# Kernel tuning notes

Measured on AMD Instinct MI355X. Metric: run time of the kernel, lower is better.

The kernel has to match this reference:

```python
import jax, jax.numpy as jnp
import numpy as np

D_MODEL = 1024
NUM_HEADS = 16
D_K = D_MODEL // NUM_HEADS


def setup_inputs() -> dict:
    key = jax.random.key(0)
    ks = jax.random.split(key, 11)
    B, S, D = 4, 2048, D_MODEL
    scale = 1.0 / np.sqrt(D)
    inp = {
        'query': jax.random.normal(ks[0], (B, S, D), jnp.float32),
        'key':   jax.random.normal(ks[1], (B, S, D), jnp.float32),
        'value': jax.random.normal(ks[2], (B, S, D), jnp.float32),
        'Wq': jax.random.normal(ks[3], (D, D), jnp.float32) * scale,
        'bq': jnp.zeros((D,), jnp.float32),
        'Wk': jax.random.normal(ks[4], (D, D), jnp.float32) * scale,
        'bk': jnp.zeros((D,), jnp.float32),
        'Wv': jax.random.normal(ks[5], (D, D), jnp.float32) * scale,
        'bv': jnp.zeros((D,), jnp.float32),
        'Wo': jax.random.normal(ks[6], (D, D), jnp.float32) * scale,
        'bo': jnp.zeros((D,), jnp.float32),
    }
    return inp


def _mha(query, key, value, Wq, bq, Wk, bk, Wv, bv, Wo, bo):
    B, S, D = query.shape
    H, dk = NUM_HEADS, D_K
    # Linear projections then split heads: [B, S, D] -> [B, H, S, dk]
    def split_heads(x):
        return x.reshape(B, S, H, dk).transpose(0, 2, 1, 3)
    Q = split_heads(query @ Wq + bq)
    K = split_heads(key @ Wk + bk)
    V = split_heads(value @ Wv + bv)
    # Scores: [B, H, S, S]
    scores = jnp.einsum('bhqd,bhkd->bhqk', Q, K) / jnp.sqrt(jnp.float32(dk)).astype(Q.dtype)
    attn = jax.nn.softmax(scores, axis=-1)
    # Context: [B, H, S, dk] -> [B, S, D]
    ctx = jnp.einsum('bhqk,bhkd->bhqd', attn, V)
    ctx = ctx.transpose(0, 2, 1, 3).reshape(B, S, D)
    return ctx @ Wo + bo


def reference(query, key, value, Wq, bq, Wk, bk, Wv, bv, Wo, bo):
    return _mha(query, key, value, Wq, bq, Wk, bk, Wv, bv, Wo, bo)
```

## Files before the change

kernel.cpp:

```cpp
#include <hip/hip_runtime.h>

typedef __attribute__((ext_vector_type(8))) short s8v;
typedef __attribute__((ext_vector_type(4))) float f4v;

#define MFMA16(a, b, c) __builtin_amdgcn_mfma_f32_16x16x32_bf16(a, b, c, 0, 0, 0)

__device__ __forceinline__ unsigned short f2bf(float f) {
    union { float f; unsigned int u; } v; v.f = f;
    unsigned int u = v.u;
    unsigned int r = (u + 0x7FFFu + ((u >> 16) & 1u)) >> 16;
    return (unsigned short)r;
}

__device__ __forceinline__ unsigned int cvt_pk_bf16(float lo, float hi) {
    unsigned int r;
    asm volatile("v_cvt_pk_bf16_f32 %0, %1, %2" : "=v"(r) : "v"(lo), "v"(hi));
    return r;
}

__device__ __forceinline__ void gl16(const void* g, void* l) {
    __builtin_amdgcn_global_load_lds(
        (const __attribute__((address_space(1))) void*)g,
        (__attribute__((address_space(3))) void*)l, 16, 0, 0);
}

__global__ __launch_bounds__(256) void cvt_bf16_k(
        const float* __restrict__ X0, const float* __restrict__ X1,
        const float* __restrict__ X2,
        unsigned short* __restrict__ Y0, unsigned short* __restrict__ Y1,
        unsigned short* __restrict__ Y2) {
    const float* X; unsigned short* Y;
    switch (blockIdx.y) {
        case 0:  X = X0; Y = Y0; break;
        case 1:  X = X1; Y = Y1; break;
        default: X = X2; Y = Y2; break;
    }
    size_t i = ((size_t)blockIdx.x * 256 + threadIdx.x) * 8;
    float4 a = *reinterpret_cast<const float4*>(X + i);
    float4 b = *reinterpret_cast<const float4*>(X + i + 4);
    s8v o;
    o[0] = (short)f2bf(a.x); o[1] = (short)f2bf(a.y);
    o[2] = (short)f2bf(a.z); o[3] = (short)f2bf(a.w);
    o[4] = (short)f2bf(b.x); o[5] = (short)f2bf(b.y);
    o[6] = (short)f2bf(b.z); o[7] = (short)f2bf(b.w);
    *reinterpret_cast<s8v*>(Y + i) = o;
}

__global__ __launch_bounds__(256) void transpose_cvt_k(
        const float* __restrict__ W0, const float* __restrict__ W1,
        const float* __restrict__ W2, const float* __restrict__ W3,
        unsigned short* __restrict__ T0, unsigned short* __restrict__ T1,
        unsigned short* __restrict__ T2, unsigned short* __restrict__ T3) {
    __shared__ float tile[32][33];
    const float* W; unsigned short* T;
    switch (blockIdx.z) {
        case 0:  W = W0; T = T0; break;
        case 1:  W = W1; T = T1; break;
        case 2:  W = W2; T = T2; break;
        default: W = W3; T = T3; break;
    }
    int tx = threadIdx.x & 31, ty = threadIdx.x >> 5;
    int k0 = blockIdx.x * 32, n0 = blockIdx.y * 32;
#pragma unroll
    for (int i = 0; i < 32; i += 8)
        tile[ty + i][tx] = W[(size_t)(k0 + ty + i) * 1024 + n0 + tx];
    __syncthreads();
#pragma unroll
    for (int i = 0; i < 32; i += 8)
        T[(size_t)(n0 + ty + i) * 1024 + k0 + tx] = f2bf(tile[tx][ty + i]);
}

template <int OUT_MODE>
__global__ __launch_bounds__(256, 2) void gemm_bt_k(
        const unsigned short* __restrict__ A, const unsigned short* __restrict__ Bt,
        const float* __restrict__ bias, void* __restrict__ C) {
    constexpr int Kd = 1024, Nd = 1024;
    __shared__ __attribute__((aligned(16))) unsigned short As[128 * 32];
    __shared__ __attribute__((aligned(16))) unsigned short Bs[128 * 32];

    const int tid  = threadIdx.x;
    const int lane = tid & 63, wave = tid >> 6;
    const int g = lane >> 4, li = lane & 15;
    const int wr = wave >> 1, wc = wave & 1;
    const int row0 = blockIdx.y * 128, col0 = blockIdx.x * 128;
    const int lrow = lane >> 2, lcol = (lane & 3) * 8;

    f4v acc[4][4];
#pragma unroll
    for (int m = 0; m < 4; m++)
#pragma unroll
        for (int n = 0; n < 4; n++) acc[m][n] = (f4v){0.f, 0.f, 0.f, 0.f};

    for (int kt = 0; kt < Kd; kt += 32) {
        __syncthreads();
#pragma unroll
        for (int jj = 0; jj < 2; jj++) {
            int j = wave * 2 + jj;
            gl16(A  + (size_t)(row0 + j * 16 + lrow) * Kd + kt + lcol, &As[j * 512]);
            gl16(Bt + (size_t)(col0 + j * 16 + lrow) * Kd + kt + lcol, &Bs[j * 512]);
        }
        __syncthreads();

        s8v af[4], bf[4];
#pragma unroll
        for (int m = 0; m < 4; m++)
            af[m] = *reinterpret_cast<const s8v*>(&As[(wr * 64 + m * 16 + li) * 32 + g * 8]);
#pragma unroll
        for (int n = 0; n < 4; n++)
            bf[n] = *reinterpret_cast<const s8v*>(&Bs[(wc * 64 + n * 16 + li) * 32 + g * 8]);
        __builtin_amdgcn_s_setprio(1);
#pragma unroll
        for (int m = 0; m < 4; m++)
#pragma unroll
            for (int n = 0; n < 4; n++)
                acc[m][n] = MFMA16(af[m], bf[n], acc[m][n]);
        __builtin_amdgcn_s_setprio(0);
    }

#pragma unroll
    for (int n = 0; n < 4; n++) {
        int col = col0 + wc * 64 + n * 16 + li;
        float bv = bias[col];
#pragma unroll
        for (int m = 0; m < 4; m++) {
            int rbase = row0 + wr * 64 + m * 16 + g * 4;
            if constexpr (OUT_MODE == 2) {
                int h = col >> 6, d = col & 63;
                int b = rbase >> 11, s = rbase & 2047;
                ushort4 pk;
                pk.x = f2bf(acc[m][n][0] + bv);
                pk.y = f2bf(acc[m][n][1] + bv);
                pk.z = f2bf(acc[m][n][2] + bv);
                pk.w = f2bf(acc[m][n][3] + bv);
                *reinterpret_cast<ushort4*>(
                    (unsigned short*)C + ((((size_t)b * 16 + h) * 64 + d) * 2048 + s)) = pk;
            } else {
#pragma unroll
                for (int r = 0; r < 4; r++) {
                    float v = acc[m][n][r] + bv;
                    if constexpr (OUT_MODE == 1)
                        ((float*)C)[(size_t)(rbase + r) * Nd + col] = v;
                    else
                        ((unsigned short*)C)[(size_t)(rbase + r) * Nd + col] = f2bf(v);
                }
            }
        }
    }
}

__global__ __launch_bounds__(256, 2) void attn_k(
        const unsigned short* __restrict__ Q, const unsigned short* __restrict__ K,
        const unsigned short* __restrict__ Vt, unsigned short* __restrict__ Ctx) {
    constexpr int S = 2048, Dm = 1024, DKh = 64;
    constexpr int LDK = 72, LDV = 136, LDP = 40;
    constexpr float CEXP = 0.125f * 1.44269504f;
    __shared__ __attribute__((aligned(16))) unsigned short K_lds[128 * LDK];
    __shared__ __attribute__((aligned(16))) unsigned short V_lds[64 * LDV];
    __shared__ __attribute__((aligned(16))) unsigned short P_lds[4][32 * LDP];

    const int tid  = threadIdx.x;
    const int lane = tid & 63, wave = tid >> 6;
    const int g = lane >> 4, li = lane & 15;
    const int id = blockIdx.x;
    const int bh = (id & 7) * 8 + ((id >> 3) & 7);
    const int qp = id >> 6;
    const int b = bh >> 4, h = bh & 15;
    const size_t base  = (size_t)b * S * Dm + (size_t)h * DKh;
    const size_t vbase = (size_t)bh * DKh * S;
    const int q00 = qp * 256 + wave * 32;

    s8v qf[2][2][2];
#pragma unroll
    for (int qt = 0; qt < 2; qt++)
#pragma unroll
        for (int rb = 0; rb < 2; rb++)
#pragma unroll
            for (int ks = 0; ks < 2; ks++)
                qf[qt][rb][ks] = *reinterpret_cast<const s8v*>(
                        Q + base + (size_t)(q00 + qt * 128 + rb * 16 + li) * Dm
                           + ks * 32 + g * 8);

    f4v octx[2][2][4];
    float m_run[2][2][4], l_run[2][2][4];
#pragma unroll
    for (int qt = 0; qt < 2; qt++)
#pragma unroll
        for (int rb = 0; rb < 2; rb++) {
#pragma unroll
            for (int nb = 0; nb < 4; nb++) octx[qt][rb][nb] = (f4v){0.f, 0.f, 0.f, 0.f};
#pragma unroll
            for (int r = 0; r < 4; r++) { m_run[qt][rb][r] = -1e30f; l_run[qt][rb][r] = 0.f; }
        }

    const int rdswz = ((li >> 2) & 3) << 3;

    for (int t = 0; t < 16; t++) {
        const int kv0 = t * 128;
        __syncthreads();
#pragma unroll
        for (int i = 0; i < 4; i++) {
            int e = (i * 256 + tid) * 8;
            int s = e >> 6, d = e & 63;
            *reinterpret_cast<s8v*>(&K_lds[s * LDK + d]) =
                *reinterpret_cast<const s8v*>(K + base + (size_t)(kv0 + s) * Dm + d);
            int dv = e >> 7, sv = e & 127;
            *reinterpret_cast<s8v*>(&V_lds[dv * LDV + sv]) =
                *reinterpret_cast<const s8v*>(Vt + vbase + (size_t)dv * S + kv0 + sv);
        }
        __syncthreads();

#pragma unroll
        for (int qt = 0; qt < 2; qt++) {
            f4v sc[2][8];
#pragma unroll
            for (int rb = 0; rb < 2; rb++)
#pragma unroll
                for (int cb = 0; cb < 8; cb++) sc[rb][cb] = (f4v){0.f, 0.f, 0.f, 0.f};
            __builtin_amdgcn_s_setprio(1);
#pragma unroll
            for (int cb = 0; cb < 8; cb++) {
#pragma unroll
                for (int ks = 0; ks < 2; ks++) {
                    s8v kf = *reinterpret_cast<const s8v*>(
                            &K_lds[(cb * 16 + li) * LDK + ks * 32 + g * 8]);
                    sc[0][cb] = MFMA16(qf[qt][0][ks], kf, sc[0][cb]);
                    sc[1][cb] = MFMA16(qf[qt][1][ks], kf, sc[1][cb]);
                }
            }
            __builtin_amdgcn_s_setprio(0);

            float rsum[2][4];
#pragma unroll
            for (int rb = 0; rb < 2; rb++) {
                float rmax[4];
#pragma unroll
                for (int r = 0; r < 4; r++) {
                    float v = sc[rb][0][r];
#pragma unroll
                    for (int cb = 1; cb < 8; cb++) v = fmaxf(v, sc[rb][cb][r]);
                    rmax[r] = v * CEXP;
                }
#pragma unroll
                for (int mask = 1; mask < 16; mask <<= 1)
#pragma unroll
                    for (int r = 0; r < 4; r++)
                        rmax[r] = fmaxf(rmax[r], __shfl_xor(rmax[r], mask, 64));
#pragma unroll
                for (int r = 0; r < 4; r++) {
                    float mn = fmaxf(m_run[qt][rb][r], rmax[r]);
                    float scl = __builtin_amdgcn_exp2f(m_run[qt][rb][r] - mn);
                    m_run[qt][rb][r] = mn;
                    l_run[qt][rb][r] *= scl;
                    rsum[rb][r] = 0.f;
#pragma unroll
                    for (int nb = 0; nb < 4; nb++) octx[qt][rb][nb][r] *= scl;
                }
            }

#pragma unroll
            for (int ks = 0; ks < 4; ks++) {
#pragma unroll
                for (int rb = 0; rb < 2; rb++) {
#pragma unroll
                    for (int cc = 0; cc < 2; cc++) {
                        int cb = ks * 2 + cc;
                        float p0 = __builtin_amdgcn_exp2f(fmaf(sc[rb][cb][0], CEXP, -m_run[qt][rb][0]));
                        float p1 = __builtin_amdgcn_exp2f(fmaf(sc[rb][cb][1], CEXP, -m_run[qt][rb][1]));
                        float p2 = __builtin_amdgcn_exp2f(fmaf(sc[rb][cb][2], CEXP, -m_run[qt][rb][2]));
                        float p3 = __builtin_amdgcn_exp2f(fmaf(sc[rb][cb][3], CEXP, -m_run[qt][rb][3]));
                        rsum[rb][0] += p0; rsum[rb][1] += p1;
                        rsum[rb][2] += p2; rsum[rb][3] += p3;
                        unsigned int u01 = cvt_pk_bf16(p0, p1);
                        unsigned int u23 = cvt_pk_bf16(p2, p3);
                        int rowb = rb * 16 + g * 4;
                        int colS = (cc * 16 + li) ^ (g << 3);
                        P_lds[wave][(rowb + 0) * LDP + colS] = (unsigned short)u01;
                        P_lds[wave][(rowb + 1) * LDP + colS] = (unsigned short)(u01 >> 16);
                        P_lds[wave][(rowb + 2) * LDP + colS] = (unsigned short)u23;
                        P_lds[wave][(rowb + 3) * LDP + colS] = (unsigned short)(u23 >> 16);
                    }
                }
                s8v vf[4], pf[2];
#pragma unroll
                for (int nb = 0; nb < 4; nb++)
                    vf[nb] = *reinterpret_cast<const s8v*>(
                            &V_lds[(nb * 16 + li) * LDV + ks * 32 + g * 8]);
#pragma unroll
                for (int rb = 0; rb < 2; rb++)
                    pf[rb] = *reinterpret_cast<const s8v*>(
                            &P_lds[wave][(rb * 16 + li) * LDP + ((g * 8) ^ rdswz)]);
                __builtin_amdgcn_s_setprio(1);
#pragma unroll
                for (int rb = 0; rb < 2; rb++)
#pragma unroll
                    for (int nb = 0; nb < 4; nb++)
                        octx[qt][rb][nb] = MFMA16(pf[rb], vf[nb], octx[qt][rb][nb]);
                __builtin_amdgcn_s_setprio(0);
            }

#pragma unroll
            for (int mask = 1; mask < 16; mask <<= 1)
#pragma unroll
                for (int rb = 0; rb < 2; rb++)
#pragma unroll
                    for (int r = 0; r < 4; r++)
                        rsum[rb][r] += __shfl_xor(rsum[rb][r], mask, 64);
#pragma unroll
            for (int rb = 0; rb < 2; rb++)
#pragma unroll
                for (int r = 0; r < 4; r++) l_run[qt][rb][r] += rsum[rb][r];
        }
    }

#pragma unroll
    for (int qt = 0; qt < 2; qt++)
#pragma unroll
        for (int rb = 0; rb < 2; rb++)
#pragma unroll
            for (int r = 0; r < 4; r++) {
                float inv = 1.0f / l_run[qt][rb][r];
                int row = q00 + qt * 128 + rb * 16 + g * 4 + r;
#pragma unroll
                for (int nb = 0; nb < 4; nb++) {
                    int d = nb * 16 + li;
                    Ctx[base + (size_t)row * Dm + d] = f2bf(octx[qt][rb][nb][r] * inv);
                }
            }
}

extern "C" void kernel_launch(void* const* d_in, const int* in_sizes, int n_in,
                              void* d_out, int out_size, void* d_ws, size_t ws_size,
                              hipStream_t stream) {
    const float* query = (const float*)d_in[0];
    const float* key   = (const float*)d_in[1];
    const float* value = (const float*)d_in[2];
    const float* Wq = (const float*)d_in[3];
    const float* bq = (const float*)d_in[4];
    const float* Wk = (const float*)d_in[5];
    const float* bk = (const float*)d_in[6];
    const float* Wv = (const float*)d_in[7];
    const float* bv = (const float*)d_in[8];
    const float* Wo = (const float*)d_in[9];
    const float* bo = (const float*)d_in[10];

    unsigned short* ws = (unsigned short*)d_ws;
    const size_t MD = (size_t)8192 * 1024;
    unsigned short* Qb  = ws;
    unsigned short* Kb  = Qb + MD;
    unsigned short* Vtb = Kb + MD;
    unsigned short* Cb  = Vtb + MD;
    unsigned short* Qx  = Cb + MD;
    unsigned short* Kx  = Qx + MD;
    unsigned short* Vx  = Kx + MD;
    unsigned short* Wqt = Vx + MD;
    unsigned short* Wkt = Wqt + 1024 * 1024;
    unsigned short* Wvt = Wkt + 1024 * 1024;
    unsigned short* Wot = Wvt + 1024 * 1024;

    cvt_bf16_k<<<dim3(4096, 3), 256, 0, stream>>>(query, key, value, Qx, Kx, Vx);
    transpose_cvt_k<<<dim3(32, 32, 4), 256, 0, stream>>>(Wq, Wk, Wv, Wo, Wqt, Wkt, Wvt, Wot);
    gemm_bt_k<0><<<dim3(8, 64), 256, 0, stream>>>(Qx, Wqt, bq, Qb);
    gemm_bt_k<0><<<dim3(8, 64), 256, 0, stream>>>(Kx, Wkt, bk, Kb);
    gemm_bt_k<2><<<dim3(8, 64), 256, 0, stream>>>(Vx, Wvt, bv, Vtb);
    attn_k<<<512, 256, 0, stream>>>(Qb, Kb, Vtb, Cb);
    gemm_bt_k<1><<<dim3(8, 64), 256, 0, stream>>>(Cb, Wot, bo, (float*)d_out);
}
```

Measured before the change: 300.3 us.

## Merge QKV GEMMs into one launch and shrink attention tiles for occupancy

The three projection GEMMs become one launch with blockIdx.z selecting Q, K or V, which removes launch gaps and fills more CUs (1536 blocks instead of 512 per launch). The attention kernel now gives each block 128 queries instead of 256 and steps through KV in chunks of 64 instead of 128. This doubles the grid to 1024 blocks, shrinks LDS and register use, and raises launch bounds to 4 blocks per CU to improve latency hiding. The cost is twice as many K/V tile loads per query and twice as many barriers and softmax rescale steps.

```diff
diff --git a/kernel.cpp b/kernel.cpp
--- a/kernel.cpp
+++ b/kernel.cpp
@@ -71,18 +71,15 @@
 }
 
 template <int OUT_MODE>
-__global__ __launch_bounds__(256, 2) void gemm_bt_k(
+__device__ __forceinline__ void gemm_body(
         const unsigned short* __restrict__ A, const unsigned short* __restrict__ Bt,
-        const float* __restrict__ bias, void* __restrict__ C) {
+        const float* __restrict__ bias, void* __restrict__ C,
+        unsigned short* As, unsigned short* Bs, int row0, int col0) {
     constexpr int Kd = 1024, Nd = 1024;
-    __shared__ __attribute__((aligned(16))) unsigned short As[128 * 32];
-    __shared__ __attribute__((aligned(16))) unsigned short Bs[128 * 32];
-
     const int tid  = threadIdx.x;
     const int lane = tid & 63, wave = tid >> 6;
     const int g = lane >> 4, li = lane & 15;
     const int wr = wave >> 1, wc = wave & 1;
-    const int row0 = blockIdx.y * 128, col0 = blockIdx.x * 128;
     const int lrow = lane >> 2, lcol = (lane & 3) * 8;
 
     f4v acc[4][4];
@@ -148,14 +145,42 @@
     }
 }
 
-__global__ __launch_bounds__(256, 2) void attn_k(
+__global__ __launch_bounds__(256, 2) void qkv_gemm_k(
+        const unsigned short* __restrict__ Qx, const unsigned short* __restrict__ Kx,
+        const unsigned short* __restrict__ Vx,
+        const unsigned short* __restrict__ Wqt, const unsigned short* __restrict__ Wkt,
+        const unsigned short* __restrict__ Wvt,
+        const float* __restrict__ bq, const float* __restrict__ bk,
+        const float* __restrict__ bv,
+        unsigned short* __restrict__ Qb, unsigned short* __restrict__ Kb,
+        unsigned short* __restrict__ Vtb) {
+    __shared__ __attribute__((aligned(16))) unsigned short As[128 * 32];
+    __shared__ __attribute__((aligned(16))) unsigned short Bs[128 * 32];
+    const int row0 = blockIdx.y * 128, col0 = blockIdx.x * 128;
+    switch (blockIdx.z) {
+        case 0:  gemm_body<0>(Qx, Wqt, bq, Qb,  As, Bs, row0, col0); break;
+        case 1:  gemm_body<0>(Kx, Wkt, bk, Kb,  As, Bs, row0, col0); break;
+        default: gemm_body<2>(Vx, Wvt, bv, Vtb, As, Bs, row0, col0); break;
+    }
+}
+
+__global__ __launch_bounds__(256, 2) void out_gemm_k(
+        const unsigned short* __restrict__ A, const unsigned short* __restrict__ Bt,
+        const float* __restrict__ bias, float* __restrict__ C) {
+    __shared__ __attribute__((aligned(16))) unsigned short As[128 * 32];
+    __shared__ __attribute__((aligned(16))) unsigned short Bs[128 * 32];
+    gemm_body<1>(A, Bt, bias, C, As, Bs, blockIdx.y * 128, blockIdx.x * 128);
+}
+
+__global__ __launch_bounds__(256, 4) void attn_k(
         const unsigned short* __restrict__ Q, const unsigned short* __restrict__ K,
         const unsigned short* __restrict__ Vt, unsigned short* __restrict__ Ctx) {
     constexpr int S = 2048, Dm = 1024, DKh = 64;
-    constexpr int LDK = 72, LDV = 136, LDP = 40;
+    constexpr int KVB = 64, NT = S / KVB;
+    constexpr int LDK = 72, LDV = 72, LDP = 40;
     constexpr float CEXP = 0.125f * 1.44269504f;
-    __shared__ __attribute__((aligned(16))) unsigned short K_lds[128 * LDK];
-    __shared__ __attribute__((aligned(16))) unsigned short V_lds[64 * LDV];
+    __shared__ __attribute__((aligned(16))) unsigned short K_lds[KVB * LDK];
+    __shared__ __attribute__((aligned(16))) unsigned short V_lds[DKh * LDV];
     __shared__ __attribute__((aligned(16))) unsigned short P_lds[4][32 * LDP];
 
     const int tid  = threadIdx.x;
@@ -163,169 +188,158 @@
     const int g = lane >> 4, li = lane & 15;
     const int id = blockIdx.x;
     const int bh = (id & 7) * 8 + ((id >> 3) & 7);
-    const int qp = id >> 6;
+    const int qt = id >> 6;
     const int b = bh >> 4, h = bh & 15;
+    const int q0 = qt * 128 + wave * 32;
     const size_t base  = (size_t)b * S * Dm + (size_t)h * DKh;
     const size_t vbase = (size_t)bh * DKh * S;
-    const int q00 = qp * 256 + wave * 32;
-
-    s8v qf[2][2][2];
-#pragma unroll
-    for (int qt = 0; qt < 2; qt++)
-#pragma unroll
-        for (int rb = 0; rb < 2; rb++)
-#pragma unroll
-            for (int ks = 0; ks < 2; ks++)
-                qf[qt][rb][ks] = *reinterpret_cast<const s8v*>(
-                        Q + base + (size_t)(q00 + qt * 128 + rb * 16 + li) * Dm
-                           + ks * 32 + g * 8);
-
-    f4v octx[2][2][4];
-    float m_run[2][2][4], l_run[2][2][4];
-#pragma unroll
-    for (int qt = 0; qt < 2; qt++)
-#pragma unroll
-        for (int rb = 0; rb < 2; rb++) {
-#pragma unroll
-            for (int nb = 0; nb < 4; nb++) octx[qt][rb][nb] = (f4v){0.f, 0.f, 0.f, 0.f};
-#pragma unroll
-            for (int r = 0; r < 4; r++) { m_run[qt][rb][r] = -1e30f; l_run[qt][rb][r] = 0.f; }
-        }
+
+    s8v qf[2][2];
+#pragma unroll
+    for (int rb = 0; rb < 2; rb++)
+#pragma unroll
+        for (int ks = 0; ks < 2; ks++)
+            qf[rb][ks] = *reinterpret_cast<const s8v*>(
+                    Q + base + (size_t)(q0 + rb * 16 + li) * Dm + ks * 32 + g * 8);
+
+    f4v octx[2][4];
+    float m_run[2][4], l_run[2][4];
+#pragma unroll
+    for (int rb = 0; rb < 2; rb++) {
+#pragma unroll
+        for (int nb = 0; nb < 4; nb++) octx[rb][nb] = (f4v){0.f, 0.f, 0.f, 0.f};
+#pragma unroll
+        for (int r = 0; r < 4; r++) { m_run[rb][r] = -1e30f; l_run[rb][r] = 0.f; }
+    }
 
     const int rdswz = ((li >> 2) & 3) << 3;
 
-    for (int t = 0; t < 16; t++) {
-        const int kv0 = t * 128;
+    for (int t = 0; t < NT; t++) {
+        const int kv0 = t * KVB;
         __syncthreads();
 #pragma unroll
-        for (int i = 0; i < 4; i++) {
+        for (int i = 0; i < 2; i++) {
             int e = (i * 256 + tid) * 8;
             int s = e >> 6, d = e & 63;
             *reinterpret_cast<s8v*>(&K_lds[s * LDK + d]) =
                 *reinterpret_cast<const s8v*>(K + base + (size_t)(kv0 + s) * Dm + d);
-            int dv = e >> 7, sv = e & 127;
-            *reinterpret_cast<s8v*>(&V_lds[dv * LDV + sv]) =
-                *reinterpret_cast<const s8v*>(Vt + vbase + (size_t)dv * S + kv0 + sv);
+            *reinterpret_cast<s8v*>(&V_lds[s * LDV + d]) =
+                *reinterpret_cast<const s8v*>(Vt + vbase + (size_t)s * S + kv0 + d);
         }
         __syncthreads();
 
-#pragma unroll
-        for (int qt = 0; qt < 2; qt++) {
-            f4v sc[2][8];
+        f4v sc[2][4];
+#pragma unroll
+        for (int rb = 0; rb < 2; rb++)
+#pragma unroll
+            for (int cb = 0; cb < 4; cb++) sc[rb][cb] = (f4v){0.f, 0.f, 0.f, 0.f};
+        __builtin_amdgcn_s_setprio(1);
+#pragma unroll
+        for (int cb = 0; cb < 4; cb++) {
+#pragma unroll
+            for (int ks = 0; ks < 2; ks++) {
+                s8v kf = *reinterpret_cast<const s8v*>(
+                        &K_lds[(cb * 16 + li) * LDK + ks * 32 + g * 8]);
+                sc[0][cb] = MFMA16(qf[0][ks], kf, sc[0][cb]);
+                sc[1][cb] = MFMA16(qf[1][ks], kf, sc[1][cb]);
+            }
+        }
+        __builtin_amdgcn_s_setprio(0);
+
+        float rsum[2][4];
+#pragma unroll
+        for (int rb = 0; rb < 2; rb++) {
+            float rmax[4];
+#pragma unroll
+            for (int r = 0; r < 4; r++) {
+                float v = sc[rb][0][r];
+#pragma unroll
+                for (int cb = 1; cb < 4; cb++) v = fmaxf(v, sc[rb][cb][r]);
+                rmax[r] = v * CEXP;
+            }
+#pragma unroll
+            for (int mask = 1; mask < 16; mask <<= 1)
+#pragma unroll
+                for (int r = 0; r < 4; r++)
+                    rmax[r] = fmaxf(rmax[r], __shfl_xor(rmax[r], mask, 64));
+#pragma unroll
+            for (int r = 0; r < 4; r++) {
+                float mn = fmaxf(m_run[rb][r], rmax[r]);
+                float scl = __builtin_amdgcn_exp2f(m_run[rb][r] - mn);
+                m_run[rb][r] = mn;
+                l_run[rb][r] *= scl;
+                rsum[rb][r] = 0.f;
+#pragma unroll
+                for (int nb = 0; nb < 4; nb++) octx[rb][nb][r] *= scl;
+            }
+        }
+
+#pragma unroll
+        for (int ks = 0; ks < 2; ks++) {
+#pragma unroll
+            for (int rb = 0; rb < 2; rb++) {
+#pragma unroll
+                for (int cc = 0; cc < 2; cc++) {
+                    int cb = ks * 2 + cc;
+                    float p0 = __builtin_amdgcn_exp2f(fmaf(sc[rb][cb][0], CEXP, -m_run[rb][0]));
+                    float p1 = __builtin_amdgcn_exp2f(fmaf(sc[rb][cb][1], CEXP, -m_run[rb][1]));
+                    float p2 = __builtin_amdgcn_exp2f(fmaf(sc[rb][cb][2], CEXP, -m_run[rb][2]));
+                    float p3 = __builtin_amdgcn_exp2f(fmaf(sc[rb][cb][3], CEXP, -m_run[rb][3]));
+                    rsum[rb][0] += p0; rsum[rb][1] += p1;
+                    rsum[rb][2] += p2; rsum[rb][3] += p3;
+                    unsigned int u01 = cvt_pk_bf16(p0, p1);
+                    unsigned int u23 = cvt_pk_bf16(p2, p3);
+                    int rowb = rb * 16 + g * 4;
+                    int colS = (cc * 16 + li) ^ (g << 3);
+                    P_lds[wave][(rowb + 0) * LDP + colS] = (unsigned short)u01;
+                    P_lds[wave][(rowb + 1) * LDP + colS] = (unsigned short)(u01 >> 16);
+                    P_lds[wave][(rowb + 2) * LDP + colS] = (unsigned short)u23;
+                    P_lds[wave][(rowb + 3) * LDP + colS] = (unsigned short)(u23 >> 16);
+                }
+            }
+            s8v vf[4], pf[2];
+#pragma unroll
+            for (int nb = 0; nb < 4; nb++)
+                vf[nb] = *reinterpret_cast<const s8v*>(
+                        &V_lds[(nb * 16 + li) * LDV + ks * 32 + g * 8]);
 #pragma unroll
             for (int rb = 0; rb < 2; rb++)
-#pragma unroll
-                for (int cb = 0; cb < 8; cb++) sc[rb][cb] = (f4v){0.f, 0.f, 0.f, 0.f};
+                pf[rb] = *reinterpret_cast<const s8v*>(
+                        &P_lds[wave][(rb * 16 + li) * LDP + ((g * 8) ^ rdswz)]);
             __builtin_amdgcn_s_setprio(1);
 #pragma unroll
-            for (int cb = 0; cb < 8; cb++) {
-#pragma unroll
-                for (int ks = 0; ks < 2; ks++) {
-                    s8v kf = *reinterpret_cast<const s8v*>(
-                            &K_lds[(cb * 16 + li) * LDK + ks * 32 + g * 8]);
-                    sc[0][cb] = MFMA16(qf[qt][0][ks], kf, sc[0][cb]);
-                    sc[1][cb] = MFMA16(qf[qt][1][ks], kf, sc[1][cb]);
-                }
-            }
+            for (int rb = 0; rb < 2; rb++)
+#pragma unroll
+                for (int nb = 0; nb < 4; nb++)
+                    octx[rb][nb] = MFMA16(pf[rb], vf[nb], octx[rb][nb]);
             __builtin_amdgcn_s_setprio(0);
-
-            float rsum[2][4];
-#pragma unroll
-            for (int rb = 0; rb < 2; rb++) {
-                float rmax[4];
-#pragma unroll
-                for (int r = 0; r < 4; r++) {
-                    float v = sc[rb][0][r];
-#pragma unroll
-                    for (int cb = 1; cb < 8; cb++) v = fmaxf(v, sc[rb][cb][r]);
-                    rmax[r] = v * CEXP;
-                }
-#pragma unroll
-                for (int mask = 1; mask < 16; mask <<= 1)
-#pragma unroll
-                    for (int r = 0; r < 4; r++)
-                        rmax[r] = fmaxf(rmax[r], __shfl_xor(rmax[r], mask, 64));
-#pragma unroll
-                for (int r = 0; r < 4; r++) {
-                    float mn = fmaxf(m_run[qt][rb][r], rmax[r]);
-                    float scl = __builtin_amdgcn_exp2f(m_run[qt][rb][r] - mn);
-                    m_run[qt][rb][r] = mn;
-                    l_run[qt][rb][r] *= scl;
-                    rsum[rb][r] = 0.f;
-#pragma unroll
-                    for (int nb = 0; nb < 4; nb++) octx[qt][rb][nb][r] *= scl;
-                }
-            }
-
-#pragma unroll
-            for (int ks = 0; ks < 4; ks++) {
-#pragma unroll
-                for (int rb = 0; rb < 2; rb++) {
-#pragma unroll
-                    for (int cc = 0; cc < 2; cc++) {
-                        int cb = ks * 2 + cc;
-                        float p0 = __builtin_amdgcn_exp2f(fmaf(sc[rb][cb][0], CEXP, -m_run[qt][rb][0]));
-                        float p1 = __builtin_amdgcn_exp2f(fmaf(sc[rb][cb][1], CEXP, -m_run[qt][rb][1]));
-                        float p2 = __builtin_amdgcn_exp2f(fmaf(sc[rb][cb][2], CEXP, -m_run[qt][rb][2]));
-                        float p3 = __builtin_amdgcn_exp2f(fmaf(sc[rb][cb][3], CEXP, -m_run[qt][rb][3]));
-                        rsum[rb][0] += p0; rsum[rb][1] += p1;
-                        rsum[rb][2] += p2; rsum[rb][3] += p3;
-                        unsigned int u01 = cvt_pk_bf16(p0, p1);
-                        unsigned int u23 = cvt_pk_bf16(p2, p3);
-                        int rowb = rb * 16 + g * 4;
-                        int colS = (cc * 16 + li) ^ (g << 3);
-                        P_lds[wave][(rowb + 0) * LDP + colS] = (unsigned short)u01;
-                        P_lds[wave][(rowb + 1) * LDP + colS] = (unsigned short)(u01 >> 16);
-                        P_lds[wave][(rowb + 2) * LDP + colS] = (unsigned short)u23;
-                        P_lds[wave][(rowb + 3) * LDP + colS] = (unsigned short)(u23 >> 16);
-                    }
-                }
-                s8v vf[4], pf[2];
-#pragma unroll
-                for (int nb = 0; nb < 4; nb++)
-                    vf[nb] = *reinterpret_cast<const s8v*>(
-                            &V_lds[(nb * 16 + li) * LDV + ks * 32 + g * 8]);
-#pragma unroll
-                for (int rb = 0; rb < 2; rb++)
-                    pf[rb] = *reinterpret_cast<const s8v*>(
-                            &P_lds[wave][(rb * 16 + li) * LDP + ((g * 8) ^ rdswz)]);
-                __builtin_amdgcn_s_setprio(1);
-#pragma unroll
-                for (int rb = 0; rb < 2; rb++)
-#pragma unroll
-                    for (int nb = 0; nb < 4; nb++)
-                        octx[qt][rb][nb] = MFMA16(pf[rb], vf[nb], octx[qt][rb][nb]);
-                __builtin_amdgcn_s_setprio(0);
-            }
-
-#pragma unroll
-            for (int mask = 1; mask < 16; mask <<= 1)
-#pragma unroll
-                for (int rb = 0; rb < 2; rb++)
-#pragma unroll
-                    for (int r = 0; r < 4; r++)
-                        rsum[rb][r] += __shfl_xor(rsum[rb][r], mask, 64);
+        }
+
+#pragma unroll
+        for (int mask = 1; mask < 16; mask <<= 1)
 #pragma unroll
             for (int rb = 0; rb < 2; rb++)
 #pragma unroll
-                for (int r = 0; r < 4; r++) l_run[qt][rb][r] += rsum[rb][r];
-        }
-    }
-
-#pragma unroll
-    for (int qt = 0; qt < 2; qt++)
+                for (int r = 0; r < 4; r++)
+                    rsum[rb][r] += __shfl_xor(rsum[rb][r], mask, 64);
 #pragma unroll
         for (int rb = 0; rb < 2; rb++)
 #pragma unroll
-            for (int r = 0; r < 4; r++) {
-                float inv = 1.0f / l_run[qt][rb][r];
-                int row = q00 + qt * 128 + rb * 16 + g * 4 + r;
-#pragma unroll
-                for (int nb = 0; nb < 4; nb++) {
-                    int d = nb * 16 + li;
-                    Ctx[base + (size_t)row * Dm + d] = f2bf(octx[qt][rb][nb][r] * inv);
-                }
-            }
+            for (int r = 0; r < 4; r++) l_run[rb][r] += rsum[rb][r];
+    }
+
+#pragma unroll
+    for (int rb = 0; rb < 2; rb++)
+#pragma unroll
+        for (int r = 0; r < 4; r++) {
+            float inv = 1.0f / l_run[rb][r];
+            int row = q0 + rb * 16 + g * 4 + r;
+#pragma unroll
+            for (int nb = 0; nb < 4; nb++) {
+                int d = nb * 16 + li;
+                Ctx[base + (size_t)row * Dm + d] = f2bf(octx[rb][nb][r] * inv);
+            }
+        }
 }
 
 extern "C" void kernel_launch(void* const* d_in, const int* in_sizes, int n_in,
@@ -359,9 +373,8 @@
 
     cvt_bf16_k<<<dim3(4096, 3), 256, 0, stream>>>(query, key, value, Qx, Kx, Vx);
     transpose_cvt_k<<<dim3(32, 32, 4), 256, 0, stream>>>(Wq, Wk, Wv, Wo, Wqt, Wkt, Wvt, Wot);
-    gemm_bt_k<0><<<dim3(8, 64), 256, 0, stream>>>(Qx, Wqt, bq, Qb);
-    gemm_bt_k<0><<<dim3(8, 64), 256, 0, stream>>>(Kx, Wkt, bk, Kb);
-    gemm_bt_k<2><<<dim3(8, 64), 256, 0, stream>>>(Vx, Wvt, bv, Vtb);
-    attn_k<<<512, 256, 0, stream>>>(Qb, Kb, Vtb, Cb);
-    gemm_bt_k<1><<<dim3(8, 64), 256, 0, stream>>>(Cb, Wot, bo, (float*)d_out);
-}
+    qkv_gemm_k<<<dim3(8, 64, 3), 256, 0, stream>>>(Qx, Kx, Vx, Wqt, Wkt, Wvt,
+                                                   bq, bk, bv, Qb, Kb, Vtb);
+    attn_k<<<1024, 256, 0, stream>>>(Qb, Kb, Vtb, Cb);
+    out_gemm_k<<<dim3(8, 64), 256, 0, stream>>>(Cb, Wot, bo, (float*)d_out);
+}
```

Result: slower. 342.4 us (+14.0%).
